# Performance work log

Hardware: AMD Instinct MI355X
Metric: run time of the kernel (lower is better)

## Reference

```python
import jax, jax.numpy as jnp
import numpy as np

N = 100000
E = 1600000
IN_C = 256
OUT_C = 128


def setup_inputs() -> dict:
    key = jax.random.key(0)
    k1, k2, k3 = jax.random.split(key, 3)
    x = jax.random.normal(k1, (N, IN_C), dtype=jnp.float32)
    edge_index = jax.random.randint(k2, (2, E), 0, N, dtype=jnp.int64)
    # Linear(in_channels, out_channels, bias=False): weight is [out, in]
    bound = 1.0 / np.sqrt(IN_C)
    weight = jax.random.uniform(k3, (OUT_C, IN_C), dtype=jnp.float32,
                                minval=-bound, maxval=bound)
    return {"x": x, "edge_index": edge_index, "weight": weight}


def reference(x, edge_index, weight):
    # Feature transform: x @ W.T  -> [N, OUT_C]
    h = x @ weight.T

    row, col = edge_index[0], edge_index[1]  # source, target

    # GCN normalization (add_self_loops=False, edge_weight=None -> ones)
    ones_e = jnp.ones((E,), dtype=h.dtype)
    deg = jax.ops.segment_sum(ones_e, col, num_segments=N)  # in-degree
    deg_inv_sqrt = jnp.where(deg > 0, jax.lax.rsqrt(deg), 0.0)
    ew = deg_inv_sqrt[row] * deg_inv_sqrt[col]  # [E]

    # Message passing: gather-multiply-scatter-add
    msgs = h[row] * ew[:, None]                       # [E, OUT_C]
    out = jax.ops.segment_sum(msgs, col, num_segments=N)  # [N, OUT_C]

    # Complex-to-real trick: negate second half, roll by half
    half = OUT_C // 2
    multiplier = jnp.concatenate([jnp.ones((half,), h.dtype),
                                  -jnp.ones((half,), h.dtype)])
    out = out * multiplier[None, :]
    out = jnp.roll(out, half, axis=-1)
    return out
```

## Files before the change

kernel.cpp:

```cpp
#include <hip/hip_runtime.h>
#include <hip/hip_bf16.h>

#define NN 100000
#define EE 1600000
#define INC 256
#define OUTC 128
#define NBUK 782
#define NPB  256
#define CHUNK ((EE + NPB - 1) / NPB)

typedef short bf16x8 __attribute__((ext_vector_type(8)));
typedef float f32x4 __attribute__((ext_vector_type(4)));

static __device__ __forceinline__ unsigned short f2bf(float f){
    unsigned u = __builtin_bit_cast(unsigned, f);
    u += 0x7fffu + ((u >> 16) & 1u);
    return (unsigned short)(u >> 16);
}
static __device__ __forceinline__ float bf2f(unsigned short h){
    unsigned u = ((unsigned)h) << 16;
    return __builtin_bit_cast(float, u);
}

__global__ void hist_kernel(const int* __restrict__ col, unsigned* __restrict__ bcnt){
    __shared__ unsigned h[NBUK];
    for (int i = threadIdx.x; i < NBUK; i += 256) h[i] = 0;
    __syncthreads();
    for (int i = blockIdx.x*blockDim.x + threadIdx.x; i < EE; i += gridDim.x*blockDim.x)
        atomicAdd(&h[((unsigned)col[i]) >> 7], 1u);
    __syncthreads();
    for (int i = threadIdx.x; i < NBUK; i += 256)
        if (h[i]) atomicAdd(&bcnt[i], h[i]);
}

__global__ void scanb_kernel(const unsigned* __restrict__ bcnt,
                             unsigned* __restrict__ base, unsigned* __restrict__ cursor){
    __shared__ unsigned tmp[1024];
    int t = threadIdx.x;
    unsigned v = (t < NBUK) ? bcnt[t] : 0u;
    tmp[t] = v;
    __syncthreads();
    for (int off = 1; off < 1024; off <<= 1){
        unsigned x = (t >= off) ? tmp[t-off] : 0u;
        __syncthreads();
        tmp[t] += x;
        __syncthreads();
    }
    if (t < NBUK){ unsigned ex = tmp[t] - v; base[t] = ex; cursor[t] = ex; }
    if (t == 0) base[NBUK] = EE;
}

__global__ void partition_kernel(const int* __restrict__ ei, unsigned* __restrict__ cursor,
                                 unsigned* __restrict__ packed){
    __shared__ unsigned cnt[NBUK], gpos[NBUK], cnt2[NBUK];
    int t = threadIdx.x;
    int s = blockIdx.x*CHUNK, e = min(s + CHUNK, EE);
    for (int i = t; i < NBUK; i += 256){ cnt[i] = 0; cnt2[i] = 0; }
    __syncthreads();
    for (int i = s + t; i < e; i += 256)
        atomicAdd(&cnt[((unsigned)ei[EE + i]) >> 7], 1u);
    __syncthreads();
    for (int i = t; i < NBUK; i += 256){
        unsigned c = cnt[i];
        gpos[i] = c ? atomicAdd(&cursor[i], c) : 0u;
    }
    __syncthreads();
    for (int i = s + t; i < e; i += 256){
        unsigned c = (unsigned)ei[EE + i];
        unsigned r = (unsigned)ei[i];
        unsigned b = c >> 7;
        unsigned rk = atomicAdd(&cnt2[b], 1u);
        packed[gpos[b] + rk] = ((c & 127u) << 24) | r;
    }
}

__global__ void sort_kernel(const unsigned* __restrict__ packed, const unsigned* __restrict__ base,
                            unsigned* __restrict__ erow, unsigned* __restrict__ noffs,
                            float* __restrict__ dinv){
    __shared__ unsigned cnt[128], cur[128], tmp[128];
    int t = threadIdx.x;
    unsigned s = base[blockIdx.x], e = base[blockIdx.x + 1];
    if (t < 128) cnt[t] = 0;
    __syncthreads();
    for (unsigned i = s + t; i < e; i += 256)
        atomicAdd(&cnt[packed[i] >> 24], 1u);
    __syncthreads();
    if (t < 128) tmp[t] = cnt[t];
    __syncthreads();
    for (int off = 1; off < 128; off <<= 1){
        unsigned v = (t >= off && t < 128) ? tmp[t-off] : 0u;
        __syncthreads();
        if (t < 128) tmp[t] += v;
        __syncthreads();
    }
    if (t < 128){
        unsigned ex = s + tmp[t] - cnt[t];
        cur[t] = ex;
        int node = blockIdx.x*128 + t;
        if (node < NN){
            noffs[node] = ex;
            dinv[node] = cnt[t] ? rsqrtf((float)cnt[t]) : 0.f;
        }
    }
    if (blockIdx.x == 0 && t == 0) noffs[NN] = EE;
    __syncthreads();
    for (unsigned i = s + t; i < e; i += 256){
        unsigned u = packed[i];
        unsigned pos = atomicAdd(&cur[u >> 24], 1u);
        erow[pos] = u & 0xFFFFFFu;
    }
}

__global__ void wprep_kernel(const float* __restrict__ w, unsigned short* __restrict__ wfrag){
    int idx = blockIdx.x*256 + threadIdx.x;
    if (idx < 8*8*64*8){
        int r = idx & 7, l = (idx >> 3) & 63, t = (idx >> 9) & 7, s = idx >> 12;
        int n = t*16 + (l & 15);
        int k = s*32 + ((l >> 4) << 3) + r;
        wfrag[idx] = f2bf(w[n*INC + k]);
    }
}

__launch_bounds__(256, 4)
__global__ void gemm_kernel(const float* __restrict__ x, const unsigned short* __restrict__ wfrag,
                            const float* __restrict__ dinv,
                            unsigned short* __restrict__ h2, int Nn){
    int tid = threadIdx.x;
    int wave = tid >> 6, lane = tid & 63;
    int mrow = blockIdx.x*64 + wave*16 + (lane & 15);
    const float* xr = x + (size_t)min(mrow, Nn-1) * INC;
    int kg = (lane >> 4) << 3;
    const bf16x8* wf = (const bf16x8*)wfrag;

    f32x4 acc[8];
    #pragma unroll
    for (int t = 0; t < 8; ++t) acc[t] = (f32x4){0.f,0.f,0.f,0.f};

    #pragma unroll
    for (int s = 0; s < 8; ++s){
        const float4* p = (const float4*)(xr + s*32 + kg);
        float4 a0 = p[0], a1 = p[1];
        bf16x8 af;
        af[0]=f2bf(a0.x); af[1]=f2bf(a0.y); af[2]=f2bf(a0.z); af[3]=f2bf(a0.w);
        af[4]=f2bf(a1.x); af[5]=f2bf(a1.y); af[6]=f2bf(a1.z); af[7]=f2bf(a1.w);
        #pragma unroll
        for (int t = 0; t < 8; ++t){
            bf16x8 bf = wf[(s*8 + t)*64 + lane];
            acc[t] = __builtin_amdgcn_mfma_f32_16x16x32_bf16(af, bf, acc[t], 0, 0, 0);
        }
    }

    int rbase = blockIdx.x*64 + wave*16 + ((lane >> 4) << 2);
    float sc[4];
    #pragma unroll
    for (int r = 0; r < 4; ++r){
        int row = rbase + r;
        sc[r] = (row < Nn) ? dinv[row] : 0.f;
    }
    #pragma unroll
    for (int t = 0; t < 8; ++t){
        int o  = t*16 + (lane & 15);
        int dc = (o + 64) & 127;
        float sgn = (o < 64) ? 1.f : -1.f;
        #pragma unroll
        for (int r = 0; r < 4; ++r){
            int row = rbase + r;
            if (row < Nn) h2[(size_t)row*OUTC + dc] = f2bf(sgn * sc[r] * acc[t][r]);
        }
    }
}

__launch_bounds__(256)
__global__ void gather_kernel(const unsigned short* __restrict__ h2,
                              const unsigned* __restrict__ noffs,
                              const unsigned* __restrict__ erow,
                              const float* __restrict__ dinv,
                              float* __restrict__ out, int Nn){
    int node = blockIdx.x*4 + (threadIdx.x >> 6);
    if (node >= Nn) return;
    int lane = threadIdx.x & 63;
    unsigned s = noffs[node], e = noffs[node+1];
    unsigned deg = e - s;
    const unsigned* h2u = (const unsigned*)h2;

    float lA0=0,lA1=0,lA2=0,lA3=0,lA4=0,lA5=0,lA6=0,lA7=0;
    float hA0=0,hA1=0,hA2=0,hA3=0,hA4=0,hA5=0,hA6=0,hA7=0;

    for (unsigned b = 0; b < deg; b += 64){
        unsigned my = b + lane;
        unsigned eidx = (my < deg) ? erow[s + my] : 0u;
        unsigned chunk = min(64u, deg - b);
        unsigned j = 0;
        for (; j + 8 <= chunk; j += 8){
            unsigned r0 = __shfl(eidx, (int)(j+0));
            unsigned r1 = __shfl(eidx, (int)(j+1));
            unsigned r2 = __shfl(eidx, (int)(j+2));
            unsigned r3 = __shfl(eidx, (int)(j+3));
            unsigned r4 = __shfl(eidx, (int)(j+4));
            unsigned r5 = __shfl(eidx, (int)(j+5));
            unsigned r6 = __shfl(eidx, (int)(j+6));
            unsigned r7 = __shfl(eidx, (int)(j+7));
            unsigned v0 = h2u[(size_t)r0*64 + lane];
            unsigned v1 = h2u[(size_t)r1*64 + lane];
            unsigned v2 = h2u[(size_t)r2*64 + lane];
            unsigned v3 = h2u[(size_t)r3*64 + lane];
            unsigned v4 = h2u[(size_t)r4*64 + lane];
            unsigned v5 = h2u[(size_t)r5*64 + lane];
            unsigned v6 = h2u[(size_t)r6*64 + lane];
            unsigned v7 = h2u[(size_t)r7*64 + lane];
            lA0 += bf2f((unsigned short)(v0 & 0xFFFFu)); hA0 += bf2f((unsigned short)(v0 >> 16));
            lA1 += bf2f((unsigned short)(v1 & 0xFFFFu)); hA1 += bf2f((unsigned short)(v1 >> 16));
            lA2 += bf2f((unsigned short)(v2 & 0xFFFFu)); hA2 += bf2f((unsigned short)(v2 >> 16));
            lA3 += bf2f((unsigned short)(v3 & 0xFFFFu)); hA3 += bf2f((unsigned short)(v3 >> 16));
            lA4 += bf2f((unsigned short)(v4 & 0xFFFFu)); hA4 += bf2f((unsigned short)(v4 >> 16));
            lA5 += bf2f((unsigned short)(v5 & 0xFFFFu)); hA5 += bf2f((unsigned short)(v5 >> 16));
            lA6 += bf2f((unsigned short)(v6 & 0xFFFFu)); hA6 += bf2f((unsigned short)(v6 >> 16));
            lA7 += bf2f((unsigned short)(v7 & 0xFFFFu)); hA7 += bf2f((unsigned short)(v7 >> 16));
        }
        for (; j < chunk; ++j){
            unsigned r = __shfl(eidx, (int)j);
            unsigned v = h2u[(size_t)r*64 + lane];
            lA0 += bf2f((unsigned short)(v & 0xFFFFu));
            hA0 += bf2f((unsigned short)(v >> 16));
        }
    }
    float lo = ((lA0+lA1)+(lA2+lA3)) + ((lA4+lA5)+(lA6+lA7));
    float hi = ((hA0+hA1)+(hA2+hA3)) + ((hA4+hA5)+(hA6+hA7));
    float wc = dinv[node];
    float2 o = {lo*wc, hi*wc};
    *(float2*)(out + (size_t)node*OUTC + lane*2) = o;
}

extern "C" void kernel_launch(void* const* d_in, const int* in_sizes, int n_in,
                              void* d_out, int out_size, void* d_ws, size_t ws_size,
                              hipStream_t stream){
    const float* x  = (const float*)d_in[0];
    const int*   ei = (const int*)d_in[1];
    const float* w  = (const float*)d_in[2];
    float* out = (float*)d_out;

    char* ws = (char*)d_ws;
    size_t off = 0;
    auto alloc = [&](size_t b) -> char* {
        char* p = ws + off;
        off += (b + 255) & ~(size_t)255;
        return p;
    };
    unsigned* bcnt   = (unsigned*)alloc((size_t)NBUK*4);
    unsigned* base   = (unsigned*)alloc((size_t)(NBUK+1)*4);
    unsigned* cursor = (unsigned*)alloc((size_t)NBUK*4);
    float*    dinv   = (float*)  alloc((size_t)NN*4);
    unsigned* packed = (unsigned*)alloc((size_t)EE*4);
    unsigned* erow   = (unsigned*)alloc((size_t)EE*4);
    unsigned* noffs  = (unsigned*)alloc((size_t)(NN+1)*4);
    unsigned short* wfrag = (unsigned short*)alloc((size_t)8*8*64*8*2);
    unsigned short* h2 = (unsigned short*)alloc((size_t)NN*OUTC*2);

    hipMemsetAsync(bcnt, 0, (size_t)NBUK*4, stream);
    wprep_kernel<<<128, 256, 0, stream>>>(w, wfrag);
    hist_kernel<<<256, 256, 0, stream>>>(ei + EE, bcnt);
    scanb_kernel<<<1, 1024, 0, stream>>>(bcnt, base, cursor);
    partition_kernel<<<NPB, 256, 0, stream>>>(ei, cursor, packed);
    sort_kernel<<<NBUK, 256, 0, stream>>>(packed, base, erow, noffs, dinv);
    gemm_kernel<<<(NN+63)/64, 256, 0, stream>>>(x, wfrag, dinv, h2, NN);
    gather_kernel<<<(NN+3)/4, 256, 0, stream>>>(h2, noffs, erow, dinv, out, NN);
}
```

Baseline: 162.5 us.

## Stage x tiles into swizzled LDS via direct global-to-LDS loads in GEMM

The GEMM now copies 64-row by 64-column slices of x into shared memory with global_load_lds, using an XOR swizzle on 16-byte chunks so that the later LDS reads avoid bank conflicts. Each wave then reads its A fragments from LDS instead of doing strided per-lane float4 global loads. The goal is fully coalesced global reads of x. The cost is two barriers per K-slice, no double buffering so loads and MFMAs do not overlap, and a relaxed launch bound that may change register allocation and occupancy.

```diff
diff --git a/kernel.cpp b/kernel.cpp
--- a/kernel.cpp
+++ b/kernel.cpp
@@ -121,36 +121,53 @@
     }
 }
 
-__launch_bounds__(256, 4)
+__launch_bounds__(256)
 __global__ void gemm_kernel(const float* __restrict__ x, const unsigned short* __restrict__ wfrag,
                             const float* __restrict__ dinv,
                             unsigned short* __restrict__ h2, int Nn){
+    __shared__ float xs[4096];
     int tid = threadIdx.x;
-    int wave = tid >> 6, lane = tid & 63;
-    int mrow = blockIdx.x*64 + wave*16 + (lane & 15);
-    const float* xr = x + (size_t)min(mrow, Nn-1) * INC;
-    int kg = (lane >> 4) << 3;
+    int wv = tid >> 6, lane = tid & 63;
+    int row0 = blockIdx.x*64;
+    int rrow = wv*16 + (lane & 15);
+    int kg2 = lane >> 4;
     const bf16x8* wf = (const bf16x8*)wfrag;
 
     f32x4 acc[8];
     #pragma unroll
     for (int t = 0; t < 8; ++t) acc[t] = (f32x4){0.f,0.f,0.f,0.f};
 
-    #pragma unroll
-    for (int s = 0; s < 8; ++s){
-        const float4* p = (const float4*)(xr + s*32 + kg);
-        float4 a0 = p[0], a1 = p[1];
-        bf16x8 af;
-        af[0]=f2bf(a0.x); af[1]=f2bf(a0.y); af[2]=f2bf(a0.z); af[3]=f2bf(a0.w);
-        af[4]=f2bf(a1.x); af[5]=f2bf(a1.y); af[6]=f2bf(a1.z); af[7]=f2bf(a1.w);
+    for (int sl = 0; sl < 4; ++sl){
         #pragma unroll
-        for (int t = 0; t < 8; ++t){
-            bf16x8 bf = wf[(s*8 + t)*64 + lane];
-            acc[t] = __builtin_amdgcn_mfma_f32_16x16x32_bf16(af, bf, acc[t], 0, 0, 0);
-        }
-    }
-
-    int rbase = blockIdx.x*64 + wave*16 + ((lane >> 4) << 2);
+        for (int j = 0; j < 4; ++j){
+            int L = (wv*4 + j)*64 + lane;
+            int srow = L >> 4;
+            int cslot = L & 15;
+            int kchunk = cslot ^ (srow & 15);
+            const float* g = x + (size_t)min(row0 + srow, Nn-1)*INC + sl*64 + kchunk*4;
+            __builtin_amdgcn_global_load_lds(g, &xs[(wv*4 + j)*256], 16, 0, 0);
+        }
+        __syncthreads();
+
+        #pragma unroll
+        for (int sg = 0; sg < 2; ++sg){
+            int c0 = sg*8 + kg2*2;
+            f32x4 a0 = *(const f32x4*)&xs[rrow*64 + ((c0    ) ^ (rrow & 15))*4];
+            f32x4 a1 = *(const f32x4*)&xs[rrow*64 + ((c0 + 1) ^ (rrow & 15))*4];
+            bf16x8 af;
+            af[0]=f2bf(a0[0]); af[1]=f2bf(a0[1]); af[2]=f2bf(a0[2]); af[3]=f2bf(a0[3]);
+            af[4]=f2bf(a1[0]); af[5]=f2bf(a1[1]); af[6]=f2bf(a1[2]); af[7]=f2bf(a1[3]);
+            int s = sl*2 + sg;
+            #pragma unroll
+            for (int t = 0; t < 8; ++t){
+                bf16x8 bf = wf[(s*8 + t)*64 + lane];
+                acc[t] = __builtin_amdgcn_mfma_f32_16x16x32_bf16(af, bf, acc[t], 0, 0, 0);
+            }
+        }
+        __syncthreads();
+    }
+
+    int rbase = row0 + wv*16 + ((lane >> 4) << 2);
     float sc[4];
     #pragma unroll
     for (int r = 0; r < 4; ++r){
```

Measured after the change: 165.1 us. No clear change (+1.6%).
